# Optimization experiments

Hardware: AMD Instinct MI355X
Metric: run time of the kernel (lower is better)

Reference implementation:

```python
import jax, jax.numpy as jnp
import numpy as np

N, E = 50000, 1600000
IN_DIM, HID, HEADS, DH, NCLS = 1280, 256, 4, 64, 6
NEG_SLOPE = 0.2
LN_EPS = 1e-5


def setup_inputs() -> dict:
    key = jax.random.key(0)
    ks = jax.random.split(key, 24)
    p = {}
    p['x'] = jax.random.normal(ks[0], (N, IN_DIM), dtype=jnp.float32)
    p['edge_index'] = jax.random.randint(ks[1], (2, E), 0, N, dtype=jnp.int64)
    s = 0.05
    p['W_in'] = jax.random.normal(ks[2], (IN_DIM, HID), dtype=jnp.float32) * s
    p['b_in'] = jnp.zeros((HID,), jnp.float32)
    for l in range(2):
        p[f'W_gat{l}'] = jax.random.normal(ks[3 + 6 * l], (HID, HEADS * DH), dtype=jnp.float32) * s
        p[f'att_src{l}'] = jax.random.normal(ks[4 + 6 * l], (HEADS, DH), dtype=jnp.float32) * s
        p[f'att_dst{l}'] = jax.random.normal(ks[5 + 6 * l], (HEADS, DH), dtype=jnp.float32) * s
        p[f'b_gat{l}'] = jnp.zeros((HEADS * DH,), jnp.float32)
        p[f'ln_g{l}'] = jnp.ones((HID,), jnp.float32)
        p[f'ln_b{l}'] = jnp.zeros((HID,), jnp.float32)
    p['W_c1'] = jax.random.normal(ks[20], (HID, HID // 2), dtype=jnp.float32) * s
    p['b_c1'] = jnp.zeros((HID // 2,), jnp.float32)
    p['W_c2'] = jax.random.normal(ks[21], (HID // 2, NCLS), dtype=jnp.float32) * s
    p['b_c2'] = jnp.zeros((NCLS,), jnp.float32)
    return p


def _layer_norm(h, g, b):
    mu = jnp.mean(h, axis=-1, keepdims=True)
    var = jnp.mean((h - mu) ** 2, axis=-1, keepdims=True)
    return (h - mu) * jax.lax.rsqrt(var + LN_EPS) * g + b


def _gat_conv(h, src, dst, W, a_src, a_dst, bias):
    # h: [N, HID] -> per-head projections [N, H, DH]
    xh = (h @ W).reshape(N, HEADS, DH)
    al_src = jnp.sum(xh * a_src, axis=-1)  # [N, H]
    al_dst = jnp.sum(xh * a_dst, axis=-1)  # [N, H]
    e = jax.nn.leaky_relu(al_src[src] + al_dst[dst], NEG_SLOPE)  # [E', H]
    # edge softmax over incoming edges of each destination node
    m = jax.ops.segment_max(e, dst, num_segments=N)
    e = jnp.exp(e - m[dst])
    denom = jax.ops.segment_sum(e, dst, num_segments=N)
    w = e / denom[dst]  # [E', H]
    msg = xh[src] * w[:, :, None]  # [E', H, DH]
    out = jax.ops.segment_sum(msg, dst, num_segments=N)  # [N, H, DH]
    return out.reshape(N, HEADS * DH) + bias


def reference(x, edge_index, W_in, b_in, W_gat0, att_src0, att_dst0, b_gat0, ln_g0, ln_b0,
              W_gat1, att_src1, att_dst1, b_gat1, ln_g1, ln_b1, W_c1, b_c1, W_c2, b_c2):
    # add self loops (PyG GATConv default)
    loop = jnp.arange(N, dtype=edge_index.dtype)
    src = jnp.concatenate([edge_index[0], loop])
    dst = jnp.concatenate([edge_index[1], loop])

    h = jax.nn.relu(x @ W_in + b_in)

    for (Wg, asrc, adst, bg, g, b) in ((W_gat0, att_src0, att_dst0, b_gat0, ln_g0, ln_b0),
                                       (W_gat1, att_src1, att_dst1, b_gat1, ln_g1, ln_b1)):
        h_new = _gat_conv(h, src, dst, Wg, asrc, adst, bg)
        h_new = jax.nn.relu(_layer_norm(h_new, g, b))
        h = h + h_new

    logits = jax.nn.relu(h @ W_c1 + b_c1) @ W_c2 + b_c2
    return logits
```

## Files before the change

### kernel.cpp

```cpp
#include <hip/hip_runtime.h>

#define NN 50000
#define EE 1600000
#define INDIM 1280
#define HID 256
#define HEADS 4
#define DHD 64
#define NCLS 6
#define NEG 0.2f
#define LNEPS 1e-5f

typedef __attribute__((ext_vector_type(8))) short short8;
typedef __attribute__((ext_vector_type(4))) float floatx4;

__device__ __forceinline__ unsigned short f2b(float f) {
    unsigned int u = __float_as_uint(f);
    u += 0x7FFF + ((u >> 16) & 1);
    return (unsigned short)(u >> 16);
}
__device__ __forceinline__ float b2f(unsigned short b) {
    return __uint_as_float(((unsigned int)b) << 16);
}

#define WAIT_LGKM0() __builtin_amdgcn_s_waitcnt(0xC07F)

__global__ void init_cnt_kernel(int* __restrict__ cnt) {
    int n = blockIdx.x * 256 + threadIdx.x;
    if (n < NN) cnt[n] = 1;
}

__global__ void count_edges_kernel(const int* __restrict__ dst, int* __restrict__ cnt) {
    int e = blockIdx.x * 256 + threadIdx.x;
    if (e < EE) atomicAdd(&cnt[dst[e]], 1);
}

__global__ __launch_bounds__(1024) void scan1_kernel(const int* __restrict__ cnt,
                                                     int* __restrict__ scanned,
                                                     int* __restrict__ chtot, int n) {
    __shared__ int wsum[16];
    int tid = threadIdx.x, lane = tid & 63, wv = tid >> 6;
    int i = blockIdx.x * 1024 + tid;
    int s = (i < n) ? cnt[i] : 0;
#pragma unroll
    for (int off = 1; off < 64; off <<= 1) {
        int t = __shfl_up(s, off, 64);
        if (lane >= off) s += t;
    }
    if (lane == 63) wsum[wv] = s;
    __syncthreads();
    if (tid < 16) {
        int ws = wsum[tid];
#pragma unroll
        for (int off = 1; off < 16; off <<= 1) {
            int t = __shfl_up(ws, off, 16);
            if (tid >= off) ws += t;
        }
        wsum[tid] = ws;
    }
    __syncthreads();
    s += (wv > 0) ? wsum[wv - 1] : 0;
    if (i < n) scanned[i] = s;
    if (tid == 1023) chtot[blockIdx.x] = s;
}

__global__ void scan2_kernel(int* __restrict__ chtot, int nch) {
    int lane = threadIdx.x;
    int v = (lane < nch) ? chtot[lane] : 0;
#pragma unroll
    for (int off = 1; off < 64; off <<= 1) {
        int t = __shfl_up(v, off, 64);
        if (lane >= off) v += t;
    }
    if (lane < nch) chtot[lane] = v;
}

__global__ void scan3_kernel(const int* __restrict__ scanned, const int* __restrict__ chtot,
                             int* __restrict__ rowptr, int n) {
    int i = blockIdx.x * 256 + threadIdx.x;
    if (i == 0) rowptr[0] = 0;
    if (i < n) {
        int ch = i >> 10;
        rowptr[i + 1] = scanned[i] + (ch ? chtot[ch - 1] : 0);
    }
}

__global__ void copyfill_kernel(const int* __restrict__ rowptr, int* __restrict__ cursor,
                                int* __restrict__ csr) {
    int n = blockIdx.x * 256 + threadIdx.x;
    if (n < NN) {
        int p = rowptr[n];
        csr[p] = n;
        cursor[n] = p + 1;
    }
}

__global__ void scatter_edges_kernel(const int* __restrict__ src, const int* __restrict__ dst,
                                     int* __restrict__ cursor, int* __restrict__ csr) {
    int e = blockIdx.x * 256 + threadIdx.x;
    if (e < EE) {
        int d = dst[e];
        int pos = atomicAdd(&cursor[d], 1);
        csr[pos] = src[e];
    }
}

__global__ void pack_w_kernel(const float* __restrict__ W, unsigned short* __restrict__ out,
                              int K, int N) {
    int idx = blockIdx.x * 256 + threadIdx.x;
    int total = (K >> 6) * (N >> 4) * 2 * 64;
    if (idx >= total) return;
    int ln = idx & 63;
    int t = idx >> 6;
    int ks = t & 1; t >>= 1;
    int NT = N >> 4;
    int nt = t % NT, kc = t / NT;
    int n = nt * 16 + (ln & 15);
    int k = kc * 64 + ks * 32 + ((ln >> 4) << 3);
    unsigned short u[8];
#pragma unroll
    for (int j = 0; j < 8; j++) u[j] = f2b(W[(size_t)(k + j) * N + n]);
    *(int4*)&out[(size_t)idx * 8] = *(const int4*)u;
}

template <int AF32, int KI, int NT, int ACT, int WF32, int WB16, int PROJ, int CLS>
__global__ __launch_bounds__(256) void pgemm_kernel(const float* __restrict__ Af,
                                                    const unsigned short* __restrict__ Ab,
                                                    const unsigned short* __restrict__ Bf,
                                                    const float* __restrict__ bias,
                                                    float* __restrict__ Cf,
                                                    unsigned short* __restrict__ Cb,
                                                    const float* __restrict__ aps,
                                                    const float* __restrict__ apd,
                                                    float* __restrict__ als,
                                                    float* __restrict__ ald,
                                                    const float* __restrict__ W2,
                                                    const float* __restrict__ b2,
                                                    float* __restrict__ out2,
                                                    int M) {
    constexpr int NW = NT / 4;
    constexpr int K = KI * 64;
    __shared__ __align__(16) unsigned short Als[2][4096];
    int tid = threadIdx.x, wv = tid >> 6, ln = tid & 63;
    int m0 = blockIdx.x * 64;

    int srow[2], scol[2];
#pragma unroll
    for (int i = 0; i < 2; i++) {
        int s = tid + i * 256;
        int r = s >> 3;
        srow[i] = min(m0 + r, M - 1);
        scol[i] = ((s & 7) ^ (r & 7)) * 8;
    }

    floatx4 acc[4][NW] = {};
    short8 breg[2][NW * 2];
    float4 af0[4], af1[4];
    int4 ai0[2], ai1[2];

    auto issueA = [&](int k, float4* af, int4* ai) {
#pragma unroll
        for (int i = 0; i < 2; i++) {
            if (AF32) {
                const float* p = Af + (size_t)srow[i] * K + k * 64 + scol[i];
                af[i * 2] = *(const float4*)p;
                af[i * 2 + 1] = *(const float4*)(p + 4);
            } else {
                ai[i] = *(const int4*)(Ab + (size_t)srow[i] * K + k * 64 + scol[i]);
            }
        }
    };
    auto issueB = [&](int k, short8* b) {
#pragma unroll
        for (int nw = 0; nw < NW; nw++)
#pragma unroll
            for (int ks = 0; ks < 2; ks++)
                b[nw * 2 + ks] = *(const short8*)(
                    Bf + ((((size_t)k * NT + (wv * NW + nw)) * 2 + ks) * 64 + ln) * 8);
    };
    auto writeA = [&](int k, const float4* af, const int4* ai) {
        unsigned short* dst = &Als[k & 1][0];
#pragma unroll
        for (int i = 0; i < 2; i++) {
            int4 v;
            if (AF32) {
                unsigned short u[8] = {f2b(af[2 * i].x), f2b(af[2 * i].y),
                                       f2b(af[2 * i].z), f2b(af[2 * i].w),
                                       f2b(af[2 * i + 1].x), f2b(af[2 * i + 1].y),
                                       f2b(af[2 * i + 1].z), f2b(af[2 * i + 1].w)};
                v = *(const int4*)u;
            } else {
                v = ai[i];
            }
            *(int4*)&dst[(tid + i * 256) * 8] = v;
        }
    };
    auto compute = [&](int k, const short8* b) {
        const unsigned short* src = &Als[k & 1][0];
#pragma unroll
        for (int ks = 0; ks < 2; ks++) {
            short8 a[4];
#pragma unroll
            for (int mt = 0; mt < 4; mt++) {
                int row = mt * 16 + (ln & 15);
                int g = ks * 4 + (ln >> 4);
                int off8 = (row >> 3) * 512 + (row & 7) * 64 + (g ^ (row & 7)) * 8;
                a[mt] = *(const short8*)&src[off8];
            }
#pragma unroll
            for (int nw = 0; nw < NW; nw++)
#pragma unroll
                for (int mt = 0; mt < 4; mt++)
                    acc[mt][nw] = __builtin_amdgcn_mfma_f32_16x16x32_bf16(
                        a[mt], b[nw * 2 + ks], acc[mt][nw], 0, 0, 0);
        }
    };

    issueA(0, af0, ai0);
    issueB(0, breg[0]);
    writeA(0, af0, ai0);
    WAIT_LGKM0();
    __builtin_amdgcn_s_barrier();

#pragma unroll
    for (int kk = 0; kk < KI / 2; kk++) {
        int k = kk * 2;
        issueA(k + 1, af1, ai1);
        issueB(k + 1, breg[1]);
        compute(k, breg[0]);
        writeA(k + 1, af1, ai1);
        WAIT_LGKM0();
        __builtin_amdgcn_s_barrier();
        if (k + 2 < KI) {
            issueA(k + 2, af0, ai0);
            issueB(k + 2, breg[0]);
        }
        compute(k + 1, breg[1]);
        if (k + 2 < KI) {
            writeA(k + 2, af0, ai0);
            WAIT_LGKM0();
            __builtin_amdgcn_s_barrier();
        }
    }

    constexpr int Nout = NT * 16;
    if constexpr (WF32 || WB16) {
#pragma unroll
        for (int mt = 0; mt < 4; mt++) {
#pragma unroll
            for (int nw = 0; nw < NW; nw++) {
                int col = (wv * NW + nw) * 16 + (ln & 15);
                int rb = m0 + mt * 16 + (ln >> 4) * 4;
                float bi = bias ? bias[col] : 0.f;
#pragma unroll
                for (int r = 0; r < 4; r++) {
                    int row = rb + r;
                    if (row < M) {
                        float v = acc[mt][nw][r] + bi;
                        if (ACT) v = fmaxf(v, 0.f);
                        if (WF32) Cf[(size_t)row * Nout + col] = v;
                        if (WB16) Cb[(size_t)row * Nout + col] = f2b(v);
                    }
                }
            }
        }
    }

    if constexpr (PROJ) {
        float avs[NW], avd[NW];
#pragma unroll
        for (int nw = 0; nw < NW; nw++) {
            int d = nw * 16 + (ln & 15);
            avs[nw] = aps[wv * DHD + d];
            avd[nw] = apd[wv * DHD + d];
        }
#pragma unroll
        for (int mt = 0; mt < 4; mt++) {
#pragma unroll
            for (int r = 0; r < 4; r++) {
                float ssum = 0.f, dsum = 0.f;
#pragma unroll
                for (int nw = 0; nw < NW; nw++) {
                    float v = acc[mt][nw][r];
                    ssum = fmaf(v, avs[nw], ssum);
                    dsum = fmaf(v, avd[nw], dsum);
                }
#pragma unroll
                for (int m = 8; m > 0; m >>= 1) {
                    ssum += __shfl_xor(ssum, m, 16);
                    dsum += __shfl_xor(dsum, m, 16);
                }
                int row = m0 + mt * 16 + (ln >> 4) * 4 + r;
                if ((ln & 15) == 0 && row < M) {
                    als[row * 4 + wv] = ssum;
                    ald[row * 4 + wv] = dsum;
                }
            }
        }
    }

    if constexpr (CLS) {
        __shared__ float cred[64][4][NCLS];
        float w2[NW][NCLS];
#pragma unroll
        for (int nw = 0; nw < NW; nw++) {
            int col = (wv * NW + nw) * 16 + (ln & 15);
#pragma unroll
            for (int c = 0; c < NCLS; c++) w2[nw][c] = W2[col * NCLS + c];
        }
#pragma unroll
        for (int mt = 0; mt < 4; mt++) {
#pragma unroll
            for (int r = 0; r < 4; r++) {
                float p[NCLS] = {};
#pragma unroll
                for (int nw = 0; nw < NW; nw++) {
                    int col = (wv * NW + nw) * 16 + (ln & 15);
                    float v = fmaxf(acc[mt][nw][r] + bias[col], 0.f);
#pragma unroll
                    for (int c = 0; c < NCLS; c++) p[c] = fmaf(v, w2[nw][c], p[c]);
                }
#pragma unroll
                for (int m = 8; m > 0; m >>= 1)
#pragma unroll
                    for (int c = 0; c < NCLS; c++) p[c] += __shfl_xor(p[c], m, 16);
                int rl = mt * 16 + (ln >> 4) * 4 + r;
                if ((ln & 15) == 0)
#pragma unroll
                    for (int c = 0; c < NCLS; c++) cred[rl][wv][c] = p[c];
            }
        }
        __syncthreads();
        for (int t = tid; t < 64 * NCLS; t += 256) {
            int row = t / NCLS, c = t % NCLS;
            if (m0 + row < M) {
                float s = cred[row][0][c] + cred[row][1][c] + cred[row][2][c] +
                          cred[row][3][c] + b2[c];
                out2[(size_t)(m0 + row) * NCLS + c] = s;
            }
        }
    }
}

__global__ __launch_bounds__(256) void agg_ln_kernel(const int* __restrict__ rowptr,
                                                     const int* __restrict__ csr,
                                                     const float* __restrict__ al_s,
                                                     const float* __restrict__ al_d,
                                                     const unsigned short* __restrict__ xhb,
                                                     const float* __restrict__ bgat,
                                                     const float* __restrict__ g,
                                                     const float* __restrict__ bb,
                                                     float* __restrict__ h,
                                                     unsigned short* __restrict__ hb) {
    int wv = threadIdx.x >> 6, ln = threadIdx.x & 63;
    int n = blockIdx.x * 4 + wv;
    if (n >= NN) return;
    int start = rowptr[n], end = rowptr[n + 1];
    int half = ln >> 5;
    int j = ln & 31;
    int head = j >> 3;
    float adh = al_d[n * 4 + head];

    float p[8] = {}, q[8] = {};
    float dsp = 0.f, dsq = 0.f;

    int i = start + half;
    for (; i + 2 < end; i += 4) {
        int s0 = csr[i], s1 = csr[i + 2];
        float e0 = al_s[s0 * 4 + head] + adh; e0 = e0 > 0.f ? e0 : NEG * e0;
        float e1 = al_s[s1 * 4 + head] + adh; e1 = e1 > 0.f ? e1 : NEG * e1;
        float w0 = __expf(e0), w1 = __expf(e1);
        dsp += w0; dsq += w1;
        short8 u0 = *(const short8*)&xhb[(size_t)s0 * HID + j * 8];
        short8 u1 = *(const short8*)&xhb[(size_t)s1 * HID + j * 8];
#pragma unroll
        for (int k = 0; k < 8; k++) {
            p[k] = fmaf(w0, b2f((unsigned short)u0[k]), p[k]);
            q[k] = fmaf(w1, b2f((unsigned short)u1[k]), q[k]);
        }
    }
    if (i < end) {
        int s0 = csr[i];
        float e0 = al_s[s0 * 4 + head] + adh; e0 = e0 > 0.f ? e0 : NEG * e0;
        float w0 = __expf(e0);
        dsp += w0;
        short8 u0 = *(const short8*)&xhb[(size_t)s0 * HID + j * 8];
#pragma unroll
        for (int k = 0; k < 8; k++) p[k] = fmaf(w0, b2f((unsigned short)u0[k]), p[k]);
    }

    float ds = dsp + dsq;
    ds += __shfl_xor(ds, 32, 64);
    float inv = 1.f / ds;

    const float4* bgp = (const float4*)&bgat[j * 8];
    float4 bg0 = bgp[0], bg1 = bgp[1];
    float bgk[8] = {bg0.x, bg0.y, bg0.z, bg0.w, bg1.x, bg1.y, bg1.z, bg1.w};

    float vv[8];
    float ps = 0.f, ps2 = 0.f;
#pragma unroll
    for (int k = 0; k < 8; k++) {
        float t = p[k] + q[k];
        t += __shfl_xor(t, 32, 64);
        float val = t * inv + bgk[k];
        vv[k] = val;
        ps += val;
        ps2 = fmaf(val, val, ps2);
    }
#pragma unroll
    for (int off = 16; off > 0; off >>= 1) {
        ps += __shfl_xor(ps, off, 64);
        ps2 += __shfl_xor(ps2, off, 64);
    }
    float mu = ps * (1.f / HID);
    float var = ps2 * (1.f / HID) - mu * mu;
    float rs = rsqrtf(var + LNEPS);

    const float4* gp = (const float4*)&g[j * 8];
    const float4* bp = (const float4*)&bb[j * 8];
    float4 g0 = gp[0], g1 = gp[1];
    float4 c0 = bp[0], c1 = bp[1];
    float gk[8] = {g0.x, g0.y, g0.z, g0.w, g1.x, g1.y, g1.z, g1.w};
    float ck[8] = {c0.x, c0.y, c0.z, c0.w, c1.x, c1.y, c1.z, c1.w};

    size_t idx = (size_t)n * HID + j * 8;
    const float4* hp = (const float4*)&h[idx];
    float4 h0 = hp[0], h1 = hp[1];
    float hk[8] = {h0.x, h0.y, h0.z, h0.w, h1.x, h1.y, h1.z, h1.w};

    float nh[8];
#pragma unroll
    for (int k = 0; k < 8; k++) {
        float o = fmaxf((vv[k] - mu) * rs * gk[k] + ck[k], 0.f);
        nh[k] = hk[k] + o;
    }

    if (half == 0) {
        ((float4*)&h[idx])[0] = make_float4(nh[0], nh[1], nh[2], nh[3]);
        ((float4*)&h[idx])[1] = make_float4(nh[4], nh[5], nh[6], nh[7]);
    } else {
        unsigned short ub[8];
#pragma unroll
        for (int k = 0; k < 8; k++) ub[k] = f2b(nh[k]);
        *(int4*)&hb[idx] = *(const int4*)ub;
    }
}

extern "C" void kernel_launch(void* const* d_in, const int* in_sizes, int n_in,
                              void* d_out, int out_size, void* d_ws, size_t ws_size,
                              hipStream_t stream) {
    const float* x    = (const float*)d_in[0];
    const int*   ei   = (const int*)d_in[1];
    const float* W_in = (const float*)d_in[2];
    const float* b_in = (const float*)d_in[3];
    const float* W_gat[2]   = {(const float*)d_in[4],  (const float*)d_in[10]};
    const float* att_src[2] = {(const float*)d_in[5],  (const float*)d_in[11]};
    const float* att_dst[2] = {(const float*)d_in[6],  (const float*)d_in[12]};
    const float* b_gat[2]   = {(const float*)d_in[7],  (const float*)d_in[13]};
    const float* ln_g[2]    = {(const float*)d_in[8],  (const float*)d_in[14]};
    const float* ln_b[2]    = {(const float*)d_in[9],  (const float*)d_in[15]};
    const float* W_c1 = (const float*)d_in[16];
    const float* b_c1 = (const float*)d_in[17];
    const float* W_c2 = (const float*)d_in[18];
    const float* b_c2 = (const float*)d_in[19];

    char* ws = (char*)d_ws;
    size_t off = 0;
    auto alloc = [&](size_t bytes) -> void* {
        void* p = ws + off;
        off += (bytes + 255) & ~(size_t)255;
        return p;
    };
    float*          h   = (float*)alloc((size_t)NN * HID * 4);
    unsigned short* hb  = (unsigned short*)alloc((size_t)NN * HID * 2);
    unsigned short* xhb = (unsigned short*)alloc((size_t)NN * HID * 2);
    float* al_s = (float*)alloc((size_t)NN * HEADS * 4);
    float* al_d = (float*)alloc((size_t)NN * HEADS * 4);
    int* rowptr  = (int*)alloc((size_t)(NN + 1) * 4);
    int* cursor  = (int*)alloc((size_t)NN * 4);
    int* csr     = (int*)alloc((size_t)(EE + NN) * 4);
    int* scanned = (int*)alloc((size_t)NN * 4);
    int* chtot   = (int*)alloc(64 * 4);
    unsigned short* WinF = (unsigned short*)alloc((size_t)HID * INDIM * 2);
    unsigned short* WgF0 = (unsigned short*)alloc((size_t)HID * HID * 2);
    unsigned short* WgF1 = (unsigned short*)alloc((size_t)HID * HID * 2);
    unsigned short* Wc1F = (unsigned short*)alloc((size_t)(HID / 2) * HID * 2);
    unsigned short* WgF[2] = {WgF0, WgF1};

    const int* srcv = ei;
    const int* dstv = ei + EE;

    pack_w_kernel<<<(INDIM * HID / 8 + 255) / 256, 256, 0, stream>>>(W_in, WinF, INDIM, HID);
    pack_w_kernel<<<(HID * HID / 8 + 255) / 256, 256, 0, stream>>>(W_gat[0], WgF0, HID, HID);
    pack_w_kernel<<<(HID * HID / 8 + 255) / 256, 256, 0, stream>>>(W_gat[1], WgF1, HID, HID);
    pack_w_kernel<<<(HID * (HID / 2) / 8 + 255) / 256, 256, 0, stream>>>(W_c1, Wc1F, HID, HID / 2);

    int nch = (NN + 1023) / 1024;
    init_cnt_kernel<<<(NN + 255) / 256, 256, 0, stream>>>(cursor);
    count_edges_kernel<<<(EE + 255) / 256, 256, 0, stream>>>(dstv, cursor);
    scan1_kernel<<<nch, 1024, 0, stream>>>(cursor, scanned, chtot, NN);
    scan2_kernel<<<1, 64, 0, stream>>>(chtot, nch);
    scan3_kernel<<<(NN + 255) / 256, 256, 0, stream>>>(scanned, chtot, rowptr, NN);
    copyfill_kernel<<<(NN + 255) / 256, 256, 0, stream>>>(rowptr, cursor, csr);
    scatter_edges_kernel<<<(EE + 255) / 256, 256, 0, stream>>>(srcv, dstv, cursor, csr);

    int MB64 = (NN + 63) / 64;

    pgemm_kernel<1, 20, 16, 1, 1, 1, 0, 0><<<MB64, 256, 0, stream>>>(
        x, nullptr, WinF, b_in, h, hb,
        nullptr, nullptr, nullptr, nullptr, nullptr, nullptr, nullptr, NN);

    for (int l = 0; l < 2; l++) {
        pgemm_kernel<0, 4, 16, 0, 0, 1, 1, 0><<<MB64, 256, 0, stream>>>(
            nullptr, hb, WgF[l], nullptr, nullptr, xhb,
            att_src[l], att_dst[l], al_s, al_d, nullptr, nullptr, nullptr, NN);
        agg_ln_kernel<<<(NN + 3) / 4, 256, 0, stream>>>(rowptr, csr, al_s, al_d, xhb,
                                                        b_gat[l], ln_g[l], ln_b[l], h, hb);
    }

    pgemm_kernel<0, 4, 8, 1, 0, 0, 0, 1><<<MB64, 256, 0, stream>>>(
        nullptr, hb, Wc1F, b_c1, nullptr, nullptr,
        nullptr, nullptr, nullptr, nullptr, W_c2, b_c2, (float*)d_out, NN);
}
```

Baseline: 993.1 us.

## Precompute per-edge attention weights in separate kernel and unroll aggregation by four

Adds an edge_w_kernel that computes the exponentiated leaky-relu attention weights for all edges and heads into a buffer, using a destination array recorded during CSR construction. The aggregation kernel then reads these weights directly instead of gathering al_s and computing exp inline, and its inner loop is unrolled to process four edges per half-wave for more memory-level parallelism. This trades extra global traffic (writing and reading ~26 MB of weights per layer plus an edst array) and an extra launch for a simpler gather loop.

```diff
diff --git a/kernel.cpp b/kernel.cpp
--- a/kernel.cpp
+++ b/kernel.cpp
@@ -2,6 +2,7 @@
 
 #define NN 50000
 #define EE 1600000
+#define ETOT (EE + NN)
 #define INDIM 1280
 #define HID 256
 #define HEADS 4
@@ -85,23 +86,42 @@
 }
 
 __global__ void copyfill_kernel(const int* __restrict__ rowptr, int* __restrict__ cursor,
-                                int* __restrict__ csr) {
+                                int* __restrict__ csr, int* __restrict__ edst) {
     int n = blockIdx.x * 256 + threadIdx.x;
     if (n < NN) {
         int p = rowptr[n];
         csr[p] = n;
+        edst[p] = n;
         cursor[n] = p + 1;
     }
 }
 
 __global__ void scatter_edges_kernel(const int* __restrict__ src, const int* __restrict__ dst,
-                                     int* __restrict__ cursor, int* __restrict__ csr) {
+                                     int* __restrict__ cursor, int* __restrict__ csr,
+                                     int* __restrict__ edst) {
     int e = blockIdx.x * 256 + threadIdx.x;
     if (e < EE) {
         int d = dst[e];
         int pos = atomicAdd(&cursor[d], 1);
         csr[pos] = src[e];
-    }
+        edst[pos] = d;
+    }
+}
+
+__global__ void edge_w_kernel(const int* __restrict__ csr, const int* __restrict__ edst,
+                              const float* __restrict__ al_s, const float* __restrict__ al_d,
+                              float* __restrict__ w) {
+    int e = blockIdx.x * 256 + threadIdx.x;
+    if (e >= ETOT) return;
+    int s = csr[e], d = edst[e];
+    float4 as = *(const float4*)&al_s[(size_t)s * 4];
+    float4 ad = *(const float4*)&al_d[(size_t)d * 4];
+    float e0 = as.x + ad.x; e0 = e0 > 0.f ? e0 : NEG * e0;
+    float e1 = as.y + ad.y; e1 = e1 > 0.f ? e1 : NEG * e1;
+    float e2 = as.z + ad.z; e2 = e2 > 0.f ? e2 : NEG * e2;
+    float e3 = as.w + ad.w; e3 = e3 > 0.f ? e3 : NEG * e3;
+    float4 wv = make_float4(__expf(e0), __expf(e1), __expf(e2), __expf(e3));
+    *(float4*)&w[(size_t)e * 4] = wv;
 }
 
 __global__ void pack_w_kernel(const float* __restrict__ W, unsigned short* __restrict__ out,
@@ -343,8 +363,7 @@
 
 __global__ __launch_bounds__(256) void agg_ln_kernel(const int* __restrict__ rowptr,
                                                      const int* __restrict__ csr,
-                                                     const float* __restrict__ al_s,
-                                                     const float* __restrict__ al_d,
+                                                     const float* __restrict__ wgt,
                                                      const unsigned short* __restrict__ xhb,
                                                      const float* __restrict__ bgat,
                                                      const float* __restrict__ g,
@@ -358,32 +377,39 @@
     int half = ln >> 5;
     int j = ln & 31;
     int head = j >> 3;
-    float adh = al_d[n * 4 + head];
 
     float p[8] = {}, q[8] = {};
     float dsp = 0.f, dsq = 0.f;
 
     int i = start + half;
-    for (; i + 2 < end; i += 4) {
-        int s0 = csr[i], s1 = csr[i + 2];
-        float e0 = al_s[s0 * 4 + head] + adh; e0 = e0 > 0.f ? e0 : NEG * e0;
-        float e1 = al_s[s1 * 4 + head] + adh; e1 = e1 > 0.f ? e1 : NEG * e1;
-        float w0 = __expf(e0), w1 = __expf(e1);
-        dsp += w0; dsq += w1;
+    for (; i + 6 < end; i += 8) {
+        int s0 = csr[i], s1 = csr[i + 2], s2 = csr[i + 4], s3 = csr[i + 6];
+        float w0 = wgt[(size_t)i * 4 + head];
+        float w1 = wgt[(size_t)(i + 2) * 4 + head];
+        float w2 = wgt[(size_t)(i + 4) * 4 + head];
+        float w3 = wgt[(size_t)(i + 6) * 4 + head];
         short8 u0 = *(const short8*)&xhb[(size_t)s0 * HID + j * 8];
         short8 u1 = *(const short8*)&xhb[(size_t)s1 * HID + j * 8];
+        short8 u2 = *(const short8*)&xhb[(size_t)s2 * HID + j * 8];
+        short8 u3 = *(const short8*)&xhb[(size_t)s3 * HID + j * 8];
+        dsp += w0 + w2;
+        dsq += w1 + w3;
 #pragma unroll
         for (int k = 0; k < 8; k++) {
             p[k] = fmaf(w0, b2f((unsigned short)u0[k]), p[k]);
             q[k] = fmaf(w1, b2f((unsigned short)u1[k]), q[k]);
         }
-    }
-    if (i < end) {
+#pragma unroll
+        for (int k = 0; k < 8; k++) {
+            p[k] = fmaf(w2, b2f((unsigned short)u2[k]), p[k]);
+            q[k] = fmaf(w3, b2f((unsigned short)u3[k]), q[k]);
+        }
+    }
+    for (; i < end; i += 2) {
         int s0 = csr[i];
-        float e0 = al_s[s0 * 4 + head] + adh; e0 = e0 > 0.f ? e0 : NEG * e0;
-        float w0 = __expf(e0);
+        float w0 = wgt[(size_t)i * 4 + head];
+        short8 u0 = *(const short8*)&xhb[(size_t)s0 * HID + j * 8];
         dsp += w0;
-        short8 u0 = *(const short8*)&xhb[(size_t)s0 * HID + j * 8];
 #pragma unroll
         for (int k = 0; k < 8; k++) p[k] = fmaf(w0, b2f((unsigned short)u0[k]), p[k]);
     }
@@ -478,7 +504,9 @@
     float* al_d = (float*)alloc((size_t)NN * HEADS * 4);
     int* rowptr  = (int*)alloc((size_t)(NN + 1) * 4);
     int* cursor  = (int*)alloc((size_t)NN * 4);
-    int* csr     = (int*)alloc((size_t)(EE + NN) * 4);
+    int* csr     = (int*)alloc((size_t)ETOT * 4);
+    int* edst    = (int*)alloc((size_t)ETOT * 4);
+    float* wgt   = (float*)alloc((size_t)ETOT * HEADS * 4);
     int* scanned = (int*)alloc((size_t)NN * 4);
     int* chtot   = (int*)alloc(64 * 4);
     unsigned short* WinF = (unsigned short*)alloc((size_t)HID * INDIM * 2);
@@ -501,8 +529,8 @@
     scan1_kernel<<<nch, 1024, 0, stream>>>(cursor, scanned, chtot, NN);
     scan2_kernel<<<1, 64, 0, stream>>>(chtot, nch);
     scan3_kernel<<<(NN + 255) / 256, 256, 0, stream>>>(scanned, chtot, rowptr, NN);
-    copyfill_kernel<<<(NN + 255) / 256, 256, 0, stream>>>(rowptr, cursor, csr);
-    scatter_edges_kernel<<<(EE + 255) / 256, 256, 0, stream>>>(srcv, dstv, cursor, csr);
+    copyfill_kernel<<<(NN + 255) / 256, 256, 0, stream>>>(rowptr, cursor, csr, edst);
+    scatter_edges_kernel<<<(EE + 255) / 256, 256, 0, stream>>>(srcv, dstv, cursor, csr, edst);
 
     int MB64 = (NN + 63) / 64;
 
@@ -514,7 +542,8 @@
         pgemm_kernel<0, 4, 16, 0, 0, 1, 1, 0><<<MB64, 256, 0, stream>>>(
             nullptr, hb, WgF[l], nullptr, nullptr, xhb,
             att_src[l], att_dst[l], al_s, al_d, nullptr, nullptr, nullptr, NN);
-        agg_ln_kernel<<<(NN + 3) / 4, 256, 0, stream>>>(rowptr, csr, al_s, al_d, xhb,
+        edge_w_kernel<<<(ETOT + 255) / 256, 256, 0, stream>>>(csr, edst, al_s, al_d, wgt);
+        agg_ln_kernel<<<(NN + 3) / 4, 256, 0, stream>>>(rowptr, csr, wgt, xhb,
                                                         b_gat[l], ln_g[l], ln_b[l], h, hb);
     }
 
```

After: 1.009 ms. About the same (+1.6%).

## Add dedicated 128-row input projection GEMM kernel with deeper A prefetch

Applied to the files above, without the earlier changes.

Splits the fp32-input projection (x @ W_in) out of the generic templated GEMM into a dedicated kernel using 128-row tiles, 8x4 MFMA accumulators per wave and a two-stage-ahead global prefetch of A. Each B fragment load now serves twice as many rows, halving weight traffic per output and raising MFMA density for the largest GEMM. The cost is more registers per thread and twice the LDS per block, which may lower occupancy. The generic pgemm loses its fp32-A and fp32-output paths, and its LDS indexing is simplified.

```diff
diff --git a/kernel.cpp b/kernel.cpp
--- a/kernel.cpp
+++ b/kernel.cpp
@@ -122,12 +122,120 @@
     *(int4*)&out[(size_t)idx * 8] = *(const int4*)u;
 }
 
-template <int AF32, int KI, int NT, int ACT, int WF32, int WB16, int PROJ, int CLS>
-__global__ __launch_bounds__(256) void pgemm_kernel(const float* __restrict__ Af,
-                                                    const unsigned short* __restrict__ Ab,
+__global__ __launch_bounds__(256) void inproj_kernel(const float* __restrict__ Af,
+                                                     const unsigned short* __restrict__ Bf,
+                                                     const float* __restrict__ bias,
+                                                     float* __restrict__ Cf,
+                                                     unsigned short* __restrict__ Cb) {
+    constexpr int KI = 20;
+    __shared__ __align__(16) unsigned short Als[2][8192];
+    int tid = threadIdx.x, wv = tid >> 6, ln = tid & 63;
+    int m0 = blockIdx.x * 128;
+
+    int srow[4], scol[4];
+#pragma unroll
+    for (int i = 0; i < 4; i++) {
+        int s = tid + i * 256;
+        int r = s >> 3;
+        srow[i] = min(m0 + r, NN - 1);
+        scol[i] = ((s & 7) ^ (r & 7)) * 8;
+    }
+
+    floatx4 acc[8][4] = {};
+    short8 breg[8];
+    float4 af[8];
+
+    auto issueA = [&](int k) {
+#pragma unroll
+        for (int i = 0; i < 4; i++) {
+            const float* p = Af + (size_t)srow[i] * INDIM + k * 64 + scol[i];
+            af[i * 2] = *(const float4*)p;
+            af[i * 2 + 1] = *(const float4*)(p + 4);
+        }
+    };
+    auto issueB = [&](int k) {
+#pragma unroll
+        for (int nw = 0; nw < 4; nw++)
+#pragma unroll
+            for (int ks = 0; ks < 2; ks++)
+                breg[nw * 2 + ks] = *(const short8*)(
+                    Bf + ((((size_t)k * 16 + (wv * 4 + nw)) * 2 + ks) * 64 + ln) * 8);
+    };
+    auto writeA = [&](int k) {
+        unsigned short* dst = &Als[k & 1][0];
+#pragma unroll
+        for (int i = 0; i < 4; i++) {
+            unsigned short u[8] = {f2b(af[2 * i].x), f2b(af[2 * i].y),
+                                   f2b(af[2 * i].z), f2b(af[2 * i].w),
+                                   f2b(af[2 * i + 1].x), f2b(af[2 * i + 1].y),
+                                   f2b(af[2 * i + 1].z), f2b(af[2 * i + 1].w)};
+            *(int4*)&dst[(tid + i * 256) * 8] = *(const int4*)u;
+        }
+    };
+    auto compute = [&](int k) {
+        const unsigned short* src = &Als[k & 1][0];
+#pragma unroll
+        for (int ks = 0; ks < 2; ks++) {
+            short8 a[8];
+#pragma unroll
+            for (int mt = 0; mt < 8; mt++) {
+                int row = mt * 16 + (ln & 15);
+                int g = ks * 4 + (ln >> 4);
+                a[mt] = *(const short8*)&src[row * 64 + (g ^ (row & 7)) * 8];
+            }
+#pragma unroll
+            for (int nw = 0; nw < 4; nw++)
+#pragma unroll
+                for (int mt = 0; mt < 8; mt++)
+                    acc[mt][nw] = __builtin_amdgcn_mfma_f32_16x16x32_bf16(
+                        a[mt], breg[nw * 2 + ks], acc[mt][nw], 0, 0, 0);
+        }
+    };
+
+    issueA(0);
+    writeA(0);
+    issueA(1);
+    issueB(0);
+    WAIT_LGKM0();
+    __builtin_amdgcn_s_barrier();
+
+    for (int k = 0; k < KI; k++) {
+        compute(k);
+        if (k + 1 < KI) {
+            issueB(k + 1);
+            writeA(k + 1);
+        }
+        if (k + 2 < KI) issueA(k + 2);
+        if (k + 1 < KI) {
+            WAIT_LGKM0();
+            __builtin_amdgcn_s_barrier();
+        }
+    }
+
+#pragma unroll
+    for (int mt = 0; mt < 8; mt++) {
+#pragma unroll
+        for (int nw = 0; nw < 4; nw++) {
+            int col = (wv * 4 + nw) * 16 + (ln & 15);
+            int rb = m0 + mt * 16 + (ln >> 4) * 4;
+            float bi = bias[col];
+#pragma unroll
+            for (int r = 0; r < 4; r++) {
+                int row = rb + r;
+                if (row < NN) {
+                    float v = fmaxf(acc[mt][nw][r] + bi, 0.f);
+                    Cf[(size_t)row * HID + col] = v;
+                    Cb[(size_t)row * HID + col] = f2b(v);
+                }
+            }
+        }
+    }
+}
+
+template <int KI, int NT, int ACT, int WB16, int PROJ, int CLS>
+__global__ __launch_bounds__(256) void pgemm_kernel(const unsigned short* __restrict__ Ab,
                                                     const unsigned short* __restrict__ Bf,
                                                     const float* __restrict__ bias,
-                                                    float* __restrict__ Cf,
                                                     unsigned short* __restrict__ Cb,
                                                     const float* __restrict__ aps,
                                                     const float* __restrict__ apd,
@@ -154,20 +262,12 @@
 
     floatx4 acc[4][NW] = {};
     short8 breg[2][NW * 2];
-    float4 af0[4], af1[4];
     int4 ai0[2], ai1[2];
 
-    auto issueA = [&](int k, float4* af, int4* ai) {
-#pragma unroll
-        for (int i = 0; i < 2; i++) {
-            if (AF32) {
-                const float* p = Af + (size_t)srow[i] * K + k * 64 + scol[i];
-                af[i * 2] = *(const float4*)p;
-                af[i * 2 + 1] = *(const float4*)(p + 4);
-            } else {
-                ai[i] = *(const int4*)(Ab + (size_t)srow[i] * K + k * 64 + scol[i]);
-            }
-        }
+    auto issueA = [&](int k, int4* ai) {
+#pragma unroll
+        for (int i = 0; i < 2; i++)
+            ai[i] = *(const int4*)(Ab + (size_t)srow[i] * K + k * 64 + scol[i]);
     };
     auto issueB = [&](int k, short8* b) {
 #pragma unroll
@@ -177,22 +277,10 @@
                 b[nw * 2 + ks] = *(const short8*)(
                     Bf + ((((size_t)k * NT + (wv * NW + nw)) * 2 + ks) * 64 + ln) * 8);
     };
-    auto writeA = [&](int k, const float4* af, const int4* ai) {
+    auto writeA = [&](int k, const int4* ai) {
         unsigned short* dst = &Als[k & 1][0];
 #pragma unroll
-        for (int i = 0; i < 2; i++) {
-            int4 v;
-            if (AF32) {
-                unsigned short u[8] = {f2b(af[2 * i].x), f2b(af[2 * i].y),
-                                       f2b(af[2 * i].z), f2b(af[2 * i].w),
-                                       f2b(af[2 * i + 1].x), f2b(af[2 * i + 1].y),
-                                       f2b(af[2 * i + 1].z), f2b(af[2 * i + 1].w)};
-                v = *(const int4*)u;
-            } else {
-                v = ai[i];
-            }
-            *(int4*)&dst[(tid + i * 256) * 8] = v;
-        }
+        for (int i = 0; i < 2; i++) *(int4*)&dst[(tid + i * 256) * 8] = ai[i];
     };
     auto compute = [&](int k, const short8* b) {
         const unsigned short* src = &Als[k & 1][0];
@@ -203,8 +291,7 @@
             for (int mt = 0; mt < 4; mt++) {
                 int row = mt * 16 + (ln & 15);
                 int g = ks * 4 + (ln >> 4);
-                int off8 = (row >> 3) * 512 + (row & 7) * 64 + (g ^ (row & 7)) * 8;
-                a[mt] = *(const short8*)&src[off8];
+                a[mt] = *(const short8*)&src[row * 64 + (g ^ (row & 7)) * 8];
             }
 #pragma unroll
             for (int nw = 0; nw < NW; nw++)
@@ -215,35 +302,35 @@
         }
     };
 
-    issueA(0, af0, ai0);
+    issueA(0, ai0);
     issueB(0, breg[0]);
-    writeA(0, af0, ai0);
+    writeA(0, ai0);
     WAIT_LGKM0();
     __builtin_amdgcn_s_barrier();
 
 #pragma unroll
     for (int kk = 0; kk < KI / 2; kk++) {
         int k = kk * 2;
-        issueA(k + 1, af1, ai1);
+        issueA(k + 1, ai1);
         issueB(k + 1, breg[1]);
         compute(k, breg[0]);
-        writeA(k + 1, af1, ai1);
+        writeA(k + 1, ai1);
         WAIT_LGKM0();
         __builtin_amdgcn_s_barrier();
         if (k + 2 < KI) {
-            issueA(k + 2, af0, ai0);
+            issueA(k + 2, ai0);
             issueB(k + 2, breg[0]);
         }
         compute(k + 1, breg[1]);
         if (k + 2 < KI) {
-            writeA(k + 2, af0, ai0);
+            writeA(k + 2, ai0);
             WAIT_LGKM0();
             __builtin_amdgcn_s_barrier();
         }
     }
 
     constexpr int Nout = NT * 16;
-    if constexpr (WF32 || WB16) {
+    if constexpr (WB16) {
 #pragma unroll
         for (int mt = 0; mt < 4; mt++) {
 #pragma unroll
@@ -257,8 +344,7 @@
                     if (row < M) {
                         float v = acc[mt][nw][r] + bi;
                         if (ACT) v = fmaxf(v, 0.f);
-                        if (WF32) Cf[(size_t)row * Nout + col] = v;
-                        if (WB16) Cb[(size_t)row * Nout + col] = f2b(v);
+                        Cb[(size_t)row * Nout + col] = f2b(v);
                     }
                 }
             }
@@ -504,21 +590,18 @@
     copyfill_kernel<<<(NN + 255) / 256, 256, 0, stream>>>(rowptr, cursor, csr);
     scatter_edges_kernel<<<(EE + 255) / 256, 256, 0, stream>>>(srcv, dstv, cursor, csr);
 
+    inproj_kernel<<<(NN + 127) / 128, 256, 0, stream>>>(x, WinF, b_in, h, hb);
+
     int MB64 = (NN + 63) / 64;
-
-    pgemm_kernel<1, 20, 16, 1, 1, 1, 0, 0><<<MB64, 256, 0, stream>>>(
-        x, nullptr, WinF, b_in, h, hb,
-        nullptr, nullptr, nullptr, nullptr, nullptr, nullptr, nullptr, NN);
-
     for (int l = 0; l < 2; l++) {
-        pgemm_kernel<0, 4, 16, 0, 0, 1, 1, 0><<<MB64, 256, 0, stream>>>(
-            nullptr, hb, WgF[l], nullptr, nullptr, xhb,
+        pgemm_kernel<4, 16, 0, 1, 1, 0><<<MB64, 256, 0, stream>>>(
+            hb, WgF[l], nullptr, xhb,
             att_src[l], att_dst[l], al_s, al_d, nullptr, nullptr, nullptr, NN);
         agg_ln_kernel<<<(NN + 3) / 4, 256, 0, stream>>>(rowptr, csr, al_s, al_d, xhb,
                                                         b_gat[l], ln_g[l], ln_b[l], h, hb);
     }
 
-    pgemm_kernel<0, 4, 8, 1, 0, 0, 0, 1><<<MB64, 256, 0, stream>>>(
-        nullptr, hb, Wc1F, b_c1, nullptr, nullptr,
+    pgemm_kernel<4, 8, 1, 0, 0, 1><<<MB64, 256, 0, stream>>>(
+        hb, Wc1F, b_c1, nullptr,
         nullptr, nullptr, nullptr, nullptr, W_c2, b_c2, (float*)d_out, NN);
 }
```

Measured after the change: 991.8 us. No clear change (-0.1%).
